# Optimization experiments

Measured on AMD Instinct MI355X. Metric: run time of the kernel, lower is better.

Reference implementation:

```python
import jax, jax.numpy as jnp
import numpy as np

B, S, D, H = 4, 2048, 1024, 16
HD = D // H  # head_dim = 64


def setup_inputs() -> dict:
    key = jax.random.key(0)
    ks = jax.random.split(key, 9)
    s = 1.0 / np.sqrt(D)
    return {
        "x": jax.random.normal(ks[0], (B, S, D), dtype=jnp.float32),
        "wq": jax.random.uniform(ks[1], (D, D), jnp.float32, -s, s),
        "bq": jax.random.uniform(ks[2], (D,), jnp.float32, -s, s),
        "wk": jax.random.uniform(ks[3], (D, D), jnp.float32, -s, s),
        "bk": jax.random.uniform(ks[4], (D,), jnp.float32, -s, s),
        "wv": jax.random.uniform(ks[5], (D, D), jnp.float32, -s, s),
        "bv": jax.random.uniform(ks[6], (D,), jnp.float32, -s, s),
        "wo": jax.random.uniform(ks[7], (D, D), jnp.float32, -s, s),
        "bo": jax.random.uniform(ks[8], (D,), jnp.float32, -s, s),
    }


def reference(x, wq, bq, wk, bk, wv, bv, wo, bo):
    b, s, _ = x.shape
    # projections (torch Linear: y = x @ W.T + b)
    q = (x @ wq.T + bq).reshape(b, s, H, HD).transpose(0, 2, 1, 3)  # [B,H,S,HD]
    k = (x @ wk.T + bk).reshape(b, s, H, HD).transpose(0, 2, 1, 3)
    v = (x @ wv.T + bv).reshape(b, s, H, HD).transpose(0, 2, 1, 3)
    scores = jnp.einsum("bhqd,bhkd->bhqk", q, k) / jnp.sqrt(jnp.float32(HD))
    attn = jax.nn.softmax(scores, axis=-1)  # full [B,H,S,S] as in original
    ctx = jnp.einsum("bhqk,bhkd->bhqd", attn, v)
    ctx = ctx.transpose(0, 2, 1, 3).reshape(b, s, D)
    return ctx @ wo.T + bo
```

## Files before the change

### kernel.cpp

```cpp
#include <hip/hip_runtime.h>
#include <stdint.h>


typedef __bf16 bf16x8 __attribute__((ext_vector_type(8)));
typedef float f32x4 __attribute__((ext_vector_type(4)));

__device__ __forceinline__ uint16_t f2bf(float f) {
  union { float f; uint32_t u; } c;
  c.f = f;
  uint32_t u = c.u + 0x7fffu + ((c.u >> 16) & 1u);
  return (uint16_t)(u >> 16);
}

__device__ __forceinline__ float exp2_hw(float x) {
#if defined(__has_builtin) && __has_builtin(__builtin_amdgcn_exp2f)
  return __builtin_amdgcn_exp2f(x);
#else
  return exp2f(x);
#endif
}

__device__ __forceinline__ uint32_t cvt_pk_bf16(float lo, float hi) {
  uint32_t r;
  asm("v_cvt_pk_bf16_f32 %0, %1, %2" : "=v"(r) : "v"(lo), "v"(hi));
  return r;
}

__device__ __forceinline__ void gload16(const void* g, void* l) {
  __builtin_amdgcn_global_load_lds(
      (const __attribute__((address_space(1))) uint32_t*)g,
      (__attribute__((address_space(3))) uint32_t*)l,
      16, 0, 0);
}

__global__ void cvt_f32_bf16(const float* __restrict__ in,
                             uint16_t* __restrict__ out, int n4) {
  int i = blockIdx.x * blockDim.x + threadIdx.x;
  if (i >= n4) return;
  float4 v = reinterpret_cast<const float4*>(in)[i];
  union { uint16_t u[4]; uint2 d; } o;
  o.u[0] = f2bf(v.x); o.u[1] = f2bf(v.y);
  o.u[2] = f2bf(v.z); o.u[3] = f2bf(v.w);
  reinterpret_cast<uint2*>(out)[i] = o.d;
}

template <int MODE>
__global__ __launch_bounds__(256, 2)
void gemm_nt(const uint16_t* __restrict__ A,
             const uint16_t* __restrict__ W0, const uint16_t* __restrict__ W1,
             const uint16_t* __restrict__ W2,
             const float* __restrict__ b0, const float* __restrict__ b1,
             const float* __restrict__ b2,
             uint16_t* __restrict__ oq, uint16_t* __restrict__ ok2,
             uint16_t* __restrict__ ovT, float* __restrict__ ofp) {
  __shared__ __align__(16) uint16_t Alds[2][128 * 32];
  __shared__ __align__(16) uint16_t Blds[2][128 * 32];

  const int tid = threadIdx.x;
  const int w = tid >> 6;
  const int l = tid & 63;
  const int wm = w >> 1, wn = w & 1;
  const int g = l >> 4, c16 = l & 15;
  const int brow = blockIdx.y * 128;
  const int bcol = blockIdx.x * 128;

  const uint16_t* Wsel = W0;
  const float* bsel = b0;
  if (MODE == 0) {
    const int which = bcol >> 10;
    Wsel = (which == 0) ? W0 : ((which == 1) ? W1 : W2);
    bsel = (which == 0) ? b0 : ((which == 1) ? b1 : b2);
  }
  const int bw = bcol & 1023;

  const int srow = l >> 2;
  const int scol = (l & 3) * 8;

  f32x4 acc[4][4];
#pragma unroll
  for (int i = 0; i < 4; ++i)
#pragma unroll
    for (int j = 0; j < 4; ++j) acc[i][j] = {0.f, 0.f, 0.f, 0.f};

#pragma unroll
  for (int i2 = 0; i2 < 2; ++i2) {
    const int c = 2 * w + i2;
    gload16(A + (size_t)(brow + c * 16 + srow) * 1024 + scol, &Alds[0][c * 512]);
    gload16(Wsel + (size_t)(bw + c * 16 + srow) * 1024 + scol, &Blds[0][c * 512]);
  }

  for (int kt = 0; kt < 32; ++kt) {
    __syncthreads();
    const int cur = kt & 1;
    if (kt + 1 < 32) {
      const int k0 = (kt + 1) * 32;
#pragma unroll
      for (int i2 = 0; i2 < 2; ++i2) {
        const int c = 2 * w + i2;
        gload16(A + (size_t)(brow + c * 16 + srow) * 1024 + k0 + scol,
                &Alds[cur ^ 1][c * 512]);
        gload16(Wsel + (size_t)(bw + c * 16 + srow) * 1024 + k0 + scol,
                &Blds[cur ^ 1][c * 512]);
      }
    }
    bf16x8 af[4], bfr[4];
#pragma unroll
    for (int i = 0; i < 4; ++i)
      af[i] = *reinterpret_cast<const bf16x8*>(
          &Alds[cur][(wm * 64 + i * 16 + c16) * 32 + g * 8]);
#pragma unroll
    for (int j = 0; j < 4; ++j)
      bfr[j] = *reinterpret_cast<const bf16x8*>(
          &Blds[cur][(wn * 64 + j * 16 + c16) * 32 + g * 8]);
#pragma unroll
    for (int i = 0; i < 4; ++i)
#pragma unroll
      for (int j = 0; j < 4; ++j)
        acc[i][j] = __builtin_amdgcn_mfma_f32_16x16x32_bf16(af[i], bfr[j],
                                                            acc[i][j], 0, 0, 0);
  }

#pragma unroll
  for (int i = 0; i < 4; ++i) {
#pragma unroll
    for (int j = 0; j < 4; ++j) {
      const int n = bcol + wn * 64 + j * 16 + c16;
      const int nn = n & 1023;
      const float bias = bsel[nn];
#pragma unroll
      for (int r = 0; r < 4; ++r) {
        const int m = brow + wm * 64 + i * 16 + g * 4 + r;
        const float val = acc[i][j][r] + bias;
        if (MODE == 0) {
          const int which = n >> 10;
          const int s = m & 2047, b = m >> 11;
          const int h = nn >> 6, hd = nn & 63;
          const size_t bh = (size_t)(b * 16 + h);
          if (which == 0)
            oq[(bh * 2048 + s) * 64 + hd] = f2bf(val * 0.18033688011112042f);
          else if (which == 1)
            ok2[(bh * 2048 + s) * 64 + hd] = f2bf(val);
          else
            ovT[(bh * 64 + hd) * 2048 + s] = f2bf(val);
        } else {
          ofp[(size_t)m * 1024 + n] = val;
        }
      }
    }
  }
}

__global__ __launch_bounds__(256, 4)
void attn_fwd(const uint16_t* __restrict__ Q, const uint16_t* __restrict__ K,
              const uint16_t* __restrict__ VT, uint16_t* __restrict__ CTX) {
  __shared__ __align__(16) uint16_t Klds[2][64 * 64];
  __shared__ __align__(16) uint16_t Vlds[2][64 * 64];

  const int tid = threadIdx.x;
  const int w = tid >> 6;
  const int l = tid & 63;
  const int g = l >> 4, c16 = l & 15;
  const int qb = blockIdx.x;
  const int bh = blockIdx.y;

  const uint16_t* qptr =
      Q + ((size_t)bh * 2048 + qb * 64 + w * 16 + c16) * 64 + g * 8;
  const bf16x8 q0 = *reinterpret_cast<const bf16x8*>(qptr);
  const bf16x8 q1 = *reinterpret_cast<const bf16x8*>(qptr + 32);

  f32x4 ctx[4];
#pragma unroll
  for (int ht = 0; ht < 4; ++ht) ctx[ht] = {0.f, 0.f, 0.f, 0.f};
  float M = -1024.0f;
  float L = 0.f;

  auto stage = [&](int kt, int buf) {
#pragma unroll
    for (int i2 = 0; i2 < 2; ++i2) {
      const int c = 2 * w + i2;
      const int lb = c * 1024 + l * 16;
      const int row = lb >> 7;
      const int so = lb ^ ((row & 7) << 4);
      const int colel = (so & 127) >> 1;
      gload16(K + ((size_t)bh * 2048 + kt * 64 + row) * 64 + colel,
              &Klds[buf][c * 512]);
      gload16(VT + ((size_t)bh * 64 + row) * 2048 + kt * 64 + colel,
              &Vlds[buf][c * 512]);
    }
  };

  stage(0, 0);

  for (int kt = 0; kt < 32; ++kt) {
    __syncthreads();
    const int cur = kt & 1;
    if (kt + 1 < 32) stage(kt + 1, cur ^ 1);
    const uint8_t* kb = reinterpret_cast<const uint8_t*>(&Klds[cur][0]);
    const uint8_t* vb = reinterpret_cast<const uint8_t*>(&Vlds[cur][0]);

    const float negM = -M;
    const f32x4 minit = {negM, negM, negM, negM};
    f32x4 sc[4];
    __builtin_amdgcn_s_setprio(1);
#pragma unroll
    for (int t = 0; t < 4; ++t) {
      const int key = ((t >> 1) << 5) + ((c16 >> 2) << 3) + ((t & 1) << 2) +
                      (c16 & 3);
      const int byt = key * 128 + g * 16;
      const int swz = (key & 7) << 4;
      const bf16x8 k0 = *reinterpret_cast<const bf16x8*>(kb + (byt ^ swz));
      const bf16x8 k1 = *reinterpret_cast<const bf16x8*>(kb + ((byt + 64) ^ swz));
      f32x4 s = __builtin_amdgcn_mfma_f32_16x16x32_bf16(k0, q0, minit, 0, 0, 0);
      sc[t] = __builtin_amdgcn_mfma_f32_16x16x32_bf16(k1, q1, s, 0, 0, 0);
    }
    __builtin_amdgcn_s_setprio(0);

    float mloc = fmaxf(fmaxf(sc[0][0], sc[0][1]), fmaxf(sc[0][2], sc[0][3]));
#pragma unroll
    for (int t = 1; t < 4; ++t)
      mloc = fmaxf(mloc,
                   fmaxf(fmaxf(sc[t][0], sc[t][1]), fmaxf(sc[t][2], sc[t][3])));
    mloc = fmaxf(mloc, __shfl_xor(mloc, 16));
    mloc = fmaxf(mloc, __shfl_xor(mloc, 32));

    float p4[4][4];
    if (__any(mloc > 8.0f)) {
      const float delta = fmaxf(mloc, 0.0f);
      const float corr = exp2_hw(-delta);
      M += delta;
      L *= corr;
#pragma unroll
      for (int ht = 0; ht < 4; ++ht)
#pragma unroll
        for (int r = 0; r < 4; ++r) ctx[ht][r] *= corr;
#pragma unroll
      for (int t = 0; t < 4; ++t)
#pragma unroll
        for (int r = 0; r < 4; ++r) p4[t][r] = exp2_hw(sc[t][r] - delta);
    } else {
#pragma unroll
      for (int t = 0; t < 4; ++t)
#pragma unroll
        for (int r = 0; r < 4; ++r) p4[t][r] = exp2_hw(sc[t][r]);
    }

#pragma unroll
    for (int t = 0; t < 4; ++t)
      L += (p4[t][0] + p4[t][1]) + (p4[t][2] + p4[t][3]);

    uint32_t pk[4][2];
#pragma unroll
    for (int t = 0; t < 4; ++t) {
      pk[t][0] = cvt_pk_bf16(p4[t][0], p4[t][1]);
      pk[t][1] = cvt_pk_bf16(p4[t][2], p4[t][3]);
    }
    union { uint32_t u[4]; bf16x8 v; } pa0, pa1;
    pa0.u[0] = pk[0][0]; pa0.u[1] = pk[0][1];
    pa0.u[2] = pk[1][0]; pa0.u[3] = pk[1][1];
    pa1.u[0] = pk[2][0]; pa1.u[1] = pk[2][1];
    pa1.u[2] = pk[3][0]; pa1.u[3] = pk[3][1];

    __builtin_amdgcn_s_setprio(1);
#pragma unroll
    for (int ht = 0; ht < 4; ++ht) {
      const int hd = ht * 16 + c16;
      const int byt = hd * 128 + g * 16;
      const int swz = (hd & 7) << 4;
      const bf16x8 v0 = *reinterpret_cast<const bf16x8*>(vb + (byt ^ swz));
      const bf16x8 v1 = *reinterpret_cast<const bf16x8*>(vb + ((byt + 64) ^ swz));
      ctx[ht] = __builtin_amdgcn_mfma_f32_16x16x32_bf16(v0, pa0.v, ctx[ht], 0, 0, 0);
      ctx[ht] = __builtin_amdgcn_mfma_f32_16x16x32_bf16(v1, pa1.v, ctx[ht], 0, 0, 0);
    }
    __builtin_amdgcn_s_setprio(0);
  }

  L += __shfl_xor(L, 16);
  L += __shfl_xor(L, 32);
  const float inv = 1.0f / L;

  const int b = bh >> 4, h = bh & 15;
  const int s = qb * 64 + w * 16 + c16;
#pragma unroll
  for (int ht = 0; ht < 4; ++ht) {
    uint2 st;
    st.x = cvt_pk_bf16(ctx[ht][0] * inv, ctx[ht][1] * inv);
    st.y = cvt_pk_bf16(ctx[ht][2] * inv, ctx[ht][3] * inv);
    *reinterpret_cast<uint2*>(
        &CTX[((size_t)b * 2048 + s) * 1024 + h * 64 + ht * 16 + 4 * g]) = st;
  }
}

extern "C" void kernel_launch(void* const* d_in, const int* in_sizes, int n_in,
                              void* d_out, int out_size, void* d_ws,
                              size_t ws_size, hipStream_t stream) {
  (void)in_sizes; (void)n_in; (void)out_size; (void)ws_size;
  const float* x = (const float*)d_in[0];
  const float* wq = (const float*)d_in[1];
  const float* bq = (const float*)d_in[2];
  const float* wk = (const float*)d_in[3];
  const float* bk = (const float*)d_in[4];
  const float* wv = (const float*)d_in[5];
  const float* bv = (const float*)d_in[6];
  const float* wo = (const float*)d_in[7];
  const float* bo = (const float*)d_in[8];
  float* out = (float*)d_out;

  uint8_t* ws = (uint8_t*)d_ws;
  uint16_t* xb   = (uint16_t*)(ws + 0);
  uint16_t* wqb  = (uint16_t*)(ws + 16777216);
  uint16_t* wkb  = (uint16_t*)(ws + 16777216 + 2097152);
  uint16_t* wvb  = (uint16_t*)(ws + 16777216 + 2 * 2097152);
  uint16_t* wob  = (uint16_t*)(ws + 16777216 + 3 * 2097152);
  uint16_t* qws  = (uint16_t*)(ws + 25165824);
  uint16_t* kws  = (uint16_t*)(ws + 25165824 + 16777216);
  uint16_t* vtws = (uint16_t*)(ws + 25165824 + 2 * 16777216);
  uint16_t* ctxw = (uint16_t*)(ws + 25165824 + 3 * 16777216);

  cvt_f32_bf16<<<8192, 256, 0, stream>>>(x, xb, 2097152);
  cvt_f32_bf16<<<1024, 256, 0, stream>>>(wq, wqb, 262144);
  cvt_f32_bf16<<<1024, 256, 0, stream>>>(wk, wkb, 262144);
  cvt_f32_bf16<<<1024, 256, 0, stream>>>(wv, wvb, 262144);
  cvt_f32_bf16<<<1024, 256, 0, stream>>>(wo, wob, 262144);

  gemm_nt<0><<<dim3(24, 64), 256, 0, stream>>>(
      xb, wqb, wkb, wvb, bq, bk, bv, qws, kws, vtws, nullptr);
  attn_fwd<<<dim3(32, 64), 256, 0, stream>>>(qws, kws, vtws, ctxw);
  gemm_nt<1><<<dim3(8, 64), 256, 0, stream>>>(
      ctxw, wob, nullptr, nullptr, bo, nullptr, nullptr, nullptr, nullptr,
      nullptr, out);
}
```

Measured before the change: 251.1 us.

## Retile attention to 32x32x16 MFMA with 64 query rows per wave

Rewrites the attention kernel so each wave handles 64 query rows (two 32-row groups) using 32x32x16 bf16 MFMAs instead of 16 rows with 16x16x32. Each K/V tile staged into LDS is now reused across 256 query rows per block rather than 64, cutting LDS and global traffic per unit of work. The grid shrinks from 32x64 to 64x8 blocks and is reordered so bh is the fast dimension. Register pressure rises, so launch bounds drop to 3 blocks per SM, and the grid of 512 blocks may leave the GPU less fully occupied.

```diff
diff --git a/kernel.cpp b/kernel.cpp
--- a/kernel.cpp
+++ b/kernel.cpp
@@ -4,6 +4,7 @@
 
 typedef __bf16 bf16x8 __attribute__((ext_vector_type(8)));
 typedef float f32x4 __attribute__((ext_vector_type(4)));
+typedef float f32x16 __attribute__((ext_vector_type(16)));
 
 __device__ __forceinline__ uint16_t f2bf(float f) {
   union { float f; uint32_t u; } c;
@@ -150,7 +151,7 @@
   }
 }
 
-__global__ __launch_bounds__(256, 4)
+__global__ __launch_bounds__(256, 3)
 void attn_fwd(const uint16_t* __restrict__ Q, const uint16_t* __restrict__ K,
               const uint16_t* __restrict__ VT, uint16_t* __restrict__ CTX) {
   __shared__ __align__(16) uint16_t Klds[2][64 * 64];
@@ -159,20 +160,33 @@
   const int tid = threadIdx.x;
   const int w = tid >> 6;
   const int l = tid & 63;
-  const int g = l >> 4, c16 = l & 15;
-  const int qb = blockIdx.x;
-  const int bh = blockIdx.y;
-
-  const uint16_t* qptr =
-      Q + ((size_t)bh * 2048 + qb * 64 + w * 16 + c16) * 64 + g * 8;
-  const bf16x8 q0 = *reinterpret_cast<const bf16x8*>(qptr);
-  const bf16x8 q1 = *reinterpret_cast<const bf16x8*>(qptr + 32);
-
-  f32x4 ctx[4];
-#pragma unroll
-  for (int ht = 0; ht < 4; ++ht) ctx[ht] = {0.f, 0.f, 0.f, 0.f};
-  float M = -1024.0f;
-  float L = 0.f;
+  const int hi = l >> 5, q5 = l & 31;
+  const int bh = blockIdx.x;
+  const int qb = blockIdx.y;
+  const int qrow_base = qb * 256 + w * 64;
+
+  const int kappa = (q5 & 3) | (((q5 >> 3) & 1) << 2) | (((q5 >> 2) & 1) << 3) |
+                    ((q5 >> 4) << 4);
+
+  bf16x8 qf[2][4];
+#pragma unroll
+  for (int grp = 0; grp < 2; ++grp) {
+    const uint16_t* qp =
+        Q + ((size_t)bh * 2048 + qrow_base + grp * 32 + q5) * 64 + 8 * hi;
+#pragma unroll
+    for (int ks = 0; ks < 4; ++ks)
+      qf[grp][ks] = *reinterpret_cast<const bf16x8*>(qp + 16 * ks);
+  }
+
+  f32x16 ctx[2][2];
+#pragma unroll
+  for (int grp = 0; grp < 2; ++grp)
+#pragma unroll
+    for (int hb = 0; hb < 2; ++hb)
+#pragma unroll
+      for (int e = 0; e < 16; ++e) ctx[grp][hb][e] = 0.f;
+  float M[2] = {-1024.0f, -1024.0f};
+  float L[2] = {0.f, 0.f};
 
   auto stage = [&](int kt, int buf) {
 #pragma unroll
@@ -189,6 +203,16 @@
     }
   };
 
+  int koff[4], voff[2][2];
+#pragma unroll
+  for (int ks = 0; ks < 4; ++ks)
+    koff[ks] = (32 * ks + 16 * hi) ^ ((kappa & 7) << 4);
+#pragma unroll
+  for (int half = 0; half < 2; ++half)
+#pragma unroll
+    for (int ks2 = 0; ks2 < 2; ++ks2)
+      voff[half][ks2] = (half * 64 + 32 * ks2 + 16 * hi) ^ ((q5 & 7) << 4);
+
   stage(0, 0);
 
   for (int kt = 0; kt < 32; ++kt) {
@@ -198,95 +222,108 @@
     const uint8_t* kb = reinterpret_cast<const uint8_t*>(&Klds[cur][0]);
     const uint8_t* vb = reinterpret_cast<const uint8_t*>(&Vlds[cur][0]);
 
-    const float negM = -M;
-    const f32x4 minit = {negM, negM, negM, negM};
-    f32x4 sc[4];
-    __builtin_amdgcn_s_setprio(1);
-#pragma unroll
-    for (int t = 0; t < 4; ++t) {
-      const int key = ((t >> 1) << 5) + ((c16 >> 2) << 3) + ((t & 1) << 2) +
-                      (c16 & 3);
-      const int byt = key * 128 + g * 16;
-      const int swz = (key & 7) << 4;
-      const bf16x8 k0 = *reinterpret_cast<const bf16x8*>(kb + (byt ^ swz));
-      const bf16x8 k1 = *reinterpret_cast<const bf16x8*>(kb + ((byt + 64) ^ swz));
-      f32x4 s = __builtin_amdgcn_mfma_f32_16x16x32_bf16(k0, q0, minit, 0, 0, 0);
-      sc[t] = __builtin_amdgcn_mfma_f32_16x16x32_bf16(k1, q1, s, 0, 0, 0);
-    }
-    __builtin_amdgcn_s_setprio(0);
-
-    float mloc = fmaxf(fmaxf(sc[0][0], sc[0][1]), fmaxf(sc[0][2], sc[0][3]));
-#pragma unroll
-    for (int t = 1; t < 4; ++t)
-      mloc = fmaxf(mloc,
-                   fmaxf(fmaxf(sc[t][0], sc[t][1]), fmaxf(sc[t][2], sc[t][3])));
-    mloc = fmaxf(mloc, __shfl_xor(mloc, 16));
-    mloc = fmaxf(mloc, __shfl_xor(mloc, 32));
-
-    float p4[4][4];
-    if (__any(mloc > 8.0f)) {
-      const float delta = fmaxf(mloc, 0.0f);
-      const float corr = exp2_hw(-delta);
-      M += delta;
-      L *= corr;
-#pragma unroll
-      for (int ht = 0; ht < 4; ++ht)
-#pragma unroll
-        for (int r = 0; r < 4; ++r) ctx[ht][r] *= corr;
-#pragma unroll
-      for (int t = 0; t < 4; ++t)
-#pragma unroll
-        for (int r = 0; r < 4; ++r) p4[t][r] = exp2_hw(sc[t][r] - delta);
-    } else {
-#pragma unroll
-      for (int t = 0; t < 4; ++t)
-#pragma unroll
-        for (int r = 0; r < 4; ++r) p4[t][r] = exp2_hw(sc[t][r]);
-    }
-
-#pragma unroll
-    for (int t = 0; t < 4; ++t)
-      L += (p4[t][0] + p4[t][1]) + (p4[t][2] + p4[t][3]);
-
-    uint32_t pk[4][2];
-#pragma unroll
-    for (int t = 0; t < 4; ++t) {
-      pk[t][0] = cvt_pk_bf16(p4[t][0], p4[t][1]);
-      pk[t][1] = cvt_pk_bf16(p4[t][2], p4[t][3]);
-    }
-    union { uint32_t u[4]; bf16x8 v; } pa0, pa1;
-    pa0.u[0] = pk[0][0]; pa0.u[1] = pk[0][1];
-    pa0.u[2] = pk[1][0]; pa0.u[3] = pk[1][1];
-    pa1.u[0] = pk[2][0]; pa1.u[1] = pk[2][1];
-    pa1.u[2] = pk[3][0]; pa1.u[3] = pk[3][1];
-
-    __builtin_amdgcn_s_setprio(1);
-#pragma unroll
-    for (int ht = 0; ht < 4; ++ht) {
-      const int hd = ht * 16 + c16;
-      const int byt = hd * 128 + g * 16;
-      const int swz = (hd & 7) << 4;
-      const bf16x8 v0 = *reinterpret_cast<const bf16x8*>(vb + (byt ^ swz));
-      const bf16x8 v1 = *reinterpret_cast<const bf16x8*>(vb + ((byt + 64) ^ swz));
-      ctx[ht] = __builtin_amdgcn_mfma_f32_16x16x32_bf16(v0, pa0.v, ctx[ht], 0, 0, 0);
-      ctx[ht] = __builtin_amdgcn_mfma_f32_16x16x32_bf16(v1, pa1.v, ctx[ht], 0, 0, 0);
-    }
-    __builtin_amdgcn_s_setprio(0);
-  }
-
-  L += __shfl_xor(L, 16);
-  L += __shfl_xor(L, 32);
-  const float inv = 1.0f / L;
+#pragma unroll
+    for (int half = 0; half < 2; ++half) {
+      bf16x8 kf[4];
+      const int krow = half * 32 + kappa;
+#pragma unroll
+      for (int ks = 0; ks < 4; ++ks)
+        kf[ks] = *reinterpret_cast<const bf16x8*>(kb + krow * 128 + koff[ks]);
+      bf16x8 vf[2][2];
+#pragma unroll
+      for (int hb = 0; hb < 2; ++hb) {
+        const int vrow = 32 * hb + q5;
+#pragma unroll
+        for (int ks2 = 0; ks2 < 2; ++ks2)
+          vf[hb][ks2] = *reinterpret_cast<const bf16x8*>(
+              vb + vrow * 128 + voff[half][ks2]);
+      }
+
+#pragma unroll
+      for (int grp = 0; grp < 2; ++grp) {
+        const float negM = -M[grp];
+        f32x16 sc;
+#pragma unroll
+        for (int e = 0; e < 16; ++e) sc[e] = negM;
+        __builtin_amdgcn_s_setprio(1);
+#pragma unroll
+        for (int ks = 0; ks < 4; ++ks)
+          sc = __builtin_amdgcn_mfma_f32_32x32x16_bf16(kf[ks], qf[grp][ks], sc,
+                                                       0, 0, 0);
+        __builtin_amdgcn_s_setprio(0);
+
+        float m0 = fmaxf(fmaxf(sc[0], sc[1]), fmaxf(sc[2], sc[3]));
+        float m1 = fmaxf(fmaxf(sc[4], sc[5]), fmaxf(sc[6], sc[7]));
+        float m2 = fmaxf(fmaxf(sc[8], sc[9]), fmaxf(sc[10], sc[11]));
+        float m3 = fmaxf(fmaxf(sc[12], sc[13]), fmaxf(sc[14], sc[15]));
+        float mloc = fmaxf(fmaxf(m0, m1), fmaxf(m2, m3));
+        mloc = fmaxf(mloc, __shfl_xor(mloc, 32));
+
+        float p[16];
+        if (__any(mloc > 8.0f)) {
+          const float delta = fmaxf(mloc, 0.0f);
+          const float corr = exp2_hw(-delta);
+          M[grp] += delta;
+          L[grp] *= corr;
+#pragma unroll
+          for (int hb = 0; hb < 2; ++hb)
+#pragma unroll
+            for (int e = 0; e < 16; ++e) ctx[grp][hb][e] *= corr;
+#pragma unroll
+          for (int e = 0; e < 16; ++e) p[e] = exp2_hw(sc[e] - delta);
+        } else {
+#pragma unroll
+          for (int e = 0; e < 16; ++e) p[e] = exp2_hw(sc[e]);
+        }
+
+        L[grp] += ((p[0] + p[1]) + (p[2] + p[3])) +
+                  ((p[4] + p[5]) + (p[6] + p[7])) +
+                  ((p[8] + p[9]) + (p[10] + p[11])) +
+                  ((p[12] + p[13]) + (p[14] + p[15]));
+
+        union { uint32_t u[4]; bf16x8 v; } pa0, pa1;
+        pa0.u[0] = cvt_pk_bf16(p[0], p[1]);
+        pa0.u[1] = cvt_pk_bf16(p[2], p[3]);
+        pa0.u[2] = cvt_pk_bf16(p[4], p[5]);
+        pa0.u[3] = cvt_pk_bf16(p[6], p[7]);
+        pa1.u[0] = cvt_pk_bf16(p[8], p[9]);
+        pa1.u[1] = cvt_pk_bf16(p[10], p[11]);
+        pa1.u[2] = cvt_pk_bf16(p[12], p[13]);
+        pa1.u[3] = cvt_pk_bf16(p[14], p[15]);
+
+        __builtin_amdgcn_s_setprio(1);
+#pragma unroll
+        for (int hb = 0; hb < 2; ++hb) {
+          ctx[grp][hb] = __builtin_amdgcn_mfma_f32_32x32x16_bf16(
+              vf[hb][0], pa0.v, ctx[grp][hb], 0, 0, 0);
+          ctx[grp][hb] = __builtin_amdgcn_mfma_f32_32x32x16_bf16(
+              vf[hb][1], pa1.v, ctx[grp][hb], 0, 0, 0);
+        }
+        __builtin_amdgcn_s_setprio(0);
+      }
+    }
+  }
 
   const int b = bh >> 4, h = bh & 15;
-  const int s = qb * 64 + w * 16 + c16;
-#pragma unroll
-  for (int ht = 0; ht < 4; ++ht) {
-    uint2 st;
-    st.x = cvt_pk_bf16(ctx[ht][0] * inv, ctx[ht][1] * inv);
-    st.y = cvt_pk_bf16(ctx[ht][2] * inv, ctx[ht][3] * inv);
-    *reinterpret_cast<uint2*>(
-        &CTX[((size_t)b * 2048 + s) * 1024 + h * 64 + ht * 16 + 4 * g]) = st;
+#pragma unroll
+  for (int grp = 0; grp < 2; ++grp) {
+    float Lt = L[grp] + __shfl_xor(L[grp], 32);
+    const float inv = 1.0f / Lt;
+    const int s = qrow_base + grp * 32 + q5;
+#pragma unroll
+    for (int hb = 0; hb < 2; ++hb) {
+#pragma unroll
+      for (int t = 0; t < 4; ++t) {
+        uint2 st;
+        st.x = cvt_pk_bf16(ctx[grp][hb][4 * t] * inv,
+                           ctx[grp][hb][4 * t + 1] * inv);
+        st.y = cvt_pk_bf16(ctx[grp][hb][4 * t + 2] * inv,
+                           ctx[grp][hb][4 * t + 3] * inv);
+        *reinterpret_cast<uint2*>(
+            &CTX[((size_t)b * 2048 + s) * 1024 + h * 64 + hb * 32 + t * 8 +
+                 hi * 4]) = st;
+      }
+    }
   }
 }
 
@@ -324,7 +361,7 @@
 
   gemm_nt<0><<<dim3(24, 64), 256, 0, stream>>>(
       xb, wqb, wkb, wvb, bq, bk, bv, qws, kws, vtws, nullptr);
-  attn_fwd<<<dim3(32, 64), 256, 0, stream>>>(qws, kws, vtws, ctxw);
+  attn_fwd<<<dim3(64, 8), 256, 0, stream>>>(qws, kws, vtws, ctxw);
   gemm_nt<1><<<dim3(8, 64), 256, 0, stream>>>(
       ctxw, wob, nullptr, nullptr, bo, nullptr, nullptr, nullptr, nullptr,
       nullptr, out);
```

After: 573.4 us. 128% more time.
